# Performance work log

Hardware: AMD Instinct MI355X
Metric: run time of the kernel (lower is better)

## Reference

```python
import jax, jax.numpy as jnp
import numpy as np

N_NODES = 100000
N_EDGES = 1600000
DROP_P = 0.5  # F.dropout default, training=True by default in the source
LRELU_SLOPE = 0.01
EPS = 1e-12


def setup_inputs() -> dict:
    key = jax.random.key(0)
    ks = jax.random.split(key, 8)
    x = jax.random.normal(ks[0], (N_NODES, 64), dtype=jnp.float32)
    edge_index = jax.random.randint(ks[1], (2, N_EDGES), 0, N_NODES, dtype=jnp.int64)
    s = 1.0 / np.sqrt(64)
    W1_l = jax.random.uniform(ks[2], (64, 32), jnp.float32, -s, s)
    W1_r = jax.random.uniform(ks[3], (64, 32), jnp.float32, -s, s)
    b1 = jnp.zeros((32,), jnp.float32)
    s2 = 1.0 / np.sqrt(32)
    W2_l = jax.random.uniform(ks[4], (32, 64), jnp.float32, -s2, s2)
    W2_r = jax.random.uniform(ks[5], (32, 64), jnp.float32, -s2, s2)
    b2 = jnp.zeros((64,), jnp.float32)
    return {"x": x, "edge_index": edge_index, "W1_l": W1_l, "b1": b1,
            "W1_r": W1_r, "W2_l": W2_l, "b2": b2, "W2_r": W2_r}


def _sage_conv(x, src, dst, W_l, b, W_r, n):
    # mean aggregation of source features onto destinations (PyG SAGEConv)
    msg = x[src]                                                 # [E, d]
    agg = jax.ops.segment_sum(msg, dst, num_segments=n)          # [N, d]
    cnt = jax.ops.segment_sum(jnp.ones((src.shape[0],), x.dtype), dst, num_segments=n)
    mean = agg / jnp.maximum(cnt, 1.0)[:, None]
    return mean @ W_l + b + x @ W_r


def _dropout(x, key):
    keep = jax.random.bernoulli(key, 1.0 - DROP_P, x.shape)
    return jnp.where(keep, x / (1.0 - DROP_P), 0.0).astype(x.dtype)


def reference(x, edge_index, W1_l, b1, W1_r, W2_l, b2, W2_r):
    n = x.shape[0]
    src, dst = edge_index[0], edge_index[1]
    dk = jax.random.split(jax.random.key(42), 2)
    h = _sage_conv(x, src, dst, W1_l, b1, W1_r, n)
    h = jax.nn.leaky_relu(h, LRELU_SLOPE)
    h = _dropout(h, dk[0])
    h = _sage_conv(h, src, dst, W2_l, b2, W2_r, n)
    h = _dropout(h, dk[1])
    norm = jnp.sqrt(jnp.sum(h * h, axis=1, keepdims=True))
    return h / jnp.maximum(norm, EPS)
```

## Files before the change

### kernel.cpp

```cpp
#include <hip/hip_runtime.h>

#define N_NODES 100000
#define N_EDGES 1600000
#define NPB 32
#define NB (N_NODES / NPB)
#define CAP 704
#define NCC 49
#define CAPA 34816
#define NFB 64
#define BPC 16
#define N16 (N_NODES * 16)
#define GHB 6250

typedef float v2f __attribute__((ext_vector_type(2)));

struct U2 { unsigned a, b; };

__host__ __device__ constexpr U2 tf2x32(unsigned k0, unsigned k1, unsigned c0, unsigned c1) {
  unsigned ks2 = k0 ^ k1 ^ 0x1BD11BDAu;
  unsigned x0 = c0 + k0, x1 = c1 + k1;
#define TFR(r) { x0 += x1; x1 = (x1 << (r)) | (x1 >> (32 - (r))); x1 ^= x0; }
  TFR(13) TFR(15) TFR(26) TFR(6)
  x0 += k1;  x1 += ks2 + 1u;
  TFR(17) TFR(29) TFR(16) TFR(24)
  x0 += ks2; x1 += k0 + 2u;
  TFR(13) TFR(15) TFR(26) TFR(6)
  x0 += k0;  x1 += k1 + 3u;
  TFR(17) TFR(29) TFR(16) TFR(24)
  x0 += k1;  x1 += ks2 + 4u;
  TFR(13) TFR(15) TFR(26) TFR(6)
  x0 += ks2; x1 += k0 + 5u;
#undef TFR
  return U2{x0, x1};
}

constexpr U2 DK0 = tf2x32(0u, 42u, 0u, 0u);
constexpr U2 DK1 = tf2x32(0u, 42u, 0u, 1u);

__device__ __forceinline__ bool keep_bit(unsigned k0, unsigned k1, unsigned j) {
  U2 w = tf2x32(k0, k1, 0u, j);
  return ((w.a ^ w.b) >> 31) == 0u;
}

__device__ __forceinline__ unsigned short f2bf(float f) {
  unsigned u = __float_as_uint(f);
  u += 0x7FFFu + ((u >> 16) & 1u);
  return (unsigned short)(u >> 16);
}
__device__ __forceinline__ v2f up2(unsigned r) {
  v2f v;
  v.x = __uint_as_float(r << 16);
  v.y = __uint_as_float(r & 0xFFFF0000u);
  return v;
}

__global__ __launch_bounds__(256, 4) void k_transform1(
    const float* __restrict__ x, const float* __restrict__ Wl,
    const float* __restrict__ Wr, unsigned short* __restrict__ xlbh,
    float* __restrict__ xr) {
  __shared__ __align__(16) float rv[4][64];
  int lane = threadIdx.x & 63;
  int wv = (threadIdx.x >> 6) & 3;
  const float* W = (lane < 32) ? Wl : Wr;
  int c = lane & 31;
  float w[64];
#pragma unroll
  for (int k = 0; k < 64; ++k) w[k] = W[k * 32 + c];
  int wid0 = (int)((blockIdx.x * blockDim.x + threadIdx.x) >> 6);
  int wstride = (int)((gridDim.x * blockDim.x) >> 6);
  for (int wid = wid0; wid < N_NODES; wid += wstride) {
    float xv = x[wid * 64 + lane];
    asm volatile("s_waitcnt lgkmcnt(0)" ::: "memory");
    rv[wv][lane] = xv;
    asm volatile("s_waitcnt lgkmcnt(0)" ::: "memory");
    v2f s0 = {0.f, 0.f}, s1 = {0.f, 0.f};
#pragma unroll
    for (int k = 0; k < 64; k += 4) {
      float4 r = *(const float4*)&rv[wv][k];
      v2f w0; w0.x = w[k + 0]; w0.y = w[k + 1];
      v2f w1; w1.x = w[k + 2]; w1.y = w[k + 3];
      v2f p0; p0.x = r.x; p0.y = r.y;
      v2f p1; p1.x = r.z; p1.y = r.w;
      s0 += p0 * w0;
      s1 += p1 * w1;
    }
    float s = (s0.x + s0.y) + (s1.x + s1.y);
    if (lane < 32) xlbh[(size_t)(c >> 4) * N16 + wid * 16 + (c & 15)] = f2bf(s);
    else           xr[wid * 32 + c] = s;
  }
}

__global__ __launch_bounds__(256) void k_binA(
    const int* __restrict__ src, const int* __restrict__ dst,
    int* __restrict__ curA, unsigned* __restrict__ bufA) {
  __shared__ int hist[NCC];
  __shared__ int offsL[NCC + 1];
  __shared__ int baseL[NCC];
  __shared__ int place[NCC];
  __shared__ unsigned stag[2048];
  __shared__ unsigned char cellb[2048];
  int t = threadIdx.x;
  for (long long start = (long long)blockIdx.x * 2048; start < N_EDGES;
       start += (long long)gridDim.x * 2048) {
    int n = (int)min((long long)2048, (long long)N_EDGES - start);
    for (int i = t; i < NCC; i += 256) hist[i] = 0;
    __syncthreads();
    unsigned pv[8]; int pc[8];
#pragma unroll
    for (int i = 0; i < 8; ++i) {
      int idx = t + i * 256;
      if (idx < n) {
        int d = dst[start + idx];
        int s = src[start + idx];
        int cc = d >> 11;
        pc[i] = cc;
        pv[i] = (unsigned)s | ((unsigned)(d & 2047) << 17);
        atomicAdd(&hist[cc], 1);
      } else pc[i] = -1;
    }
    __syncthreads();
    if (t < 64) {
      int lane = t;
      int v = (lane < NCC) ? hist[lane] : 0;
      int x = v;
#pragma unroll
      for (int o = 1; o < 64; o <<= 1) {
        int y = __shfl_up(x, o, 64);
        if (lane >= o) x += y;
      }
      if (lane < NCC) {
        offsL[lane] = x - v;
        place[lane] = 0;
        if (v > 0) baseL[lane] = atomicAdd(&curA[lane], v);
      }
      if (lane == NCC - 1) offsL[NCC] = x;
    }
    __syncthreads();
#pragma unroll
    for (int i = 0; i < 8; ++i) {
      if (pc[i] >= 0) {
        int p = atomicAdd(&place[pc[i]], 1);
        int sl = offsL[pc[i]] + p;
        stag[sl] = pv[i];
        cellb[sl] = (unsigned char)pc[i];
      }
    }
    __syncthreads();
    for (int s2 = t; s2 < n; s2 += 256) {
      int cell = cellb[s2];
      int pos = baseL[cell] + (s2 - offsL[cell]);
      if (pos < CAPA) bufA[(size_t)cell * CAPA + pos] = stag[s2];
    }
    __syncthreads();
  }
}

__global__ __launch_bounds__(256) void k_binB(
    const unsigned* __restrict__ bufA, const int* __restrict__ curA,
    int* __restrict__ cur, unsigned* __restrict__ buf) {
  __shared__ int hist[NFB];
  __shared__ int offsL[NFB + 1];
  __shared__ int baseL[NFB];
  __shared__ int place[NFB];
  __shared__ unsigned stag[2048];
  __shared__ unsigned char cellb[2048];
  int cellc = blockIdx.x / BPC;
  int slice = blockIdx.x % BPC;
  int t = threadIdx.x;
  int cnt = min(curA[cellc], CAPA);
  const unsigned* in = bufA + (size_t)cellc * CAPA;
  for (int start = slice * 2048; start < cnt; start += BPC * 2048) {
    int n = min(2048, cnt - start);
    for (int i = t; i < NFB; i += 256) hist[i] = 0;
    __syncthreads();
    unsigned pv[8]; int pb[8];
#pragma unroll
    for (int i = 0; i < 8; ++i) {
      int idx = t + i * 256;
      if (idx < n) {
        unsigned w = in[start + idx];
        int dlow = (int)(w >> 17);
        int fb = dlow >> 5;
        pb[i] = fb;
        pv[i] = (w & 0x1FFFFu) | ((unsigned)(dlow & 31) << 17);
        atomicAdd(&hist[fb], 1);
      } else pb[i] = -1;
    }
    __syncthreads();
    if (t < 64) {
      int lane = t;
      int v = hist[lane];
      int x = v;
#pragma unroll
      for (int o = 1; o < 64; o <<= 1) {
        int y = __shfl_up(x, o, 64);
        if (lane >= o) x += y;
      }
      offsL[lane] = x - v;
      place[lane] = 0;
      if (v > 0) baseL[lane] = atomicAdd(&cur[cellc * NFB + lane], v);
      if (lane == 63) offsL[NFB] = x;
    }
    __syncthreads();
#pragma unroll
    for (int i = 0; i < 8; ++i) {
      if (pb[i] >= 0) {
        int p = atomicAdd(&place[pb[i]], 1);
        int sl = offsL[pb[i]] + p;
        stag[sl] = pv[i];
        cellb[sl] = (unsigned char)pb[i];
      }
    }
    __syncthreads();
    for (int s2 = t; s2 < n; s2 += 256) {
      int fb = cellb[s2];
      int pos = baseL[fb] + (s2 - offsL[fb]);
      if (pos < CAP) buf[(size_t)(cellc * NFB + fb) * CAP + pos] = stag[s2];
    }
    __syncthreads();
  }
}

__global__ __launch_bounds__(1024) void k_bscan(
    const int* __restrict__ cur, int* __restrict__ bbase) {
  __shared__ int warp_sums[16];
  __shared__ int s_running;
  int t = threadIdx.x;
  int lane = t & 63, w = t >> 6;
  if (t == 0) s_running = 0;
  __syncthreads();
  for (int base = 0; base < NB; base += 1024) {
    int i = base + t;
    int v = (i < NB) ? min(cur[i], CAP) : 0;
    int x = v;
#pragma unroll
    for (int o = 1; o < 64; o <<= 1) {
      int y = __shfl_up(x, o, 64);
      if (lane >= o) x += y;
    }
    if (lane == 63) warp_sums[w] = x;
    __syncthreads();
    if (w == 0) {
      int ws = (lane < 16) ? warp_sums[lane] : 0;
#pragma unroll
      for (int o = 1; o < 16; o <<= 1) {
        int y = __shfl_up(ws, o, 64);
        if (lane >= o) ws += y;
      }
      if (lane < 16) warp_sums[lane] = ws;
    }
    __syncthreads();
    int incl = x + (w > 0 ? warp_sums[w - 1] : 0);
    int excl = s_running + incl - v;
    if (i < NB) bbase[i] = excl;
    __syncthreads();
    if (t == 1023) s_running += incl;
    __syncthreads();
  }
}

__global__ __launch_bounds__(256) void k_bfill(
    const unsigned* __restrict__ buf, const int* __restrict__ cur,
    const int* __restrict__ bbase, int* __restrict__ deg,
    int* __restrict__ offs, int* __restrict__ eidx) {
  __shared__ int ncnt[NPB];
  __shared__ int ncur[NPB];
  __shared__ unsigned sbuf[CAP];
  int b = blockIdx.x, t = threadIdx.x;
  if (t < NPB) ncnt[t] = 0;
  __syncthreads();
  int nb = min(cur[b], CAP);
  const unsigned* bb = buf + (size_t)b * CAP;
  for (int slot = t; slot < nb; slot += 256) {
    unsigned w = bb[slot];
    sbuf[slot] = w;
    atomicAdd(&ncnt[w >> 17], 1);
  }
  __syncthreads();
  if (t < 64) {
    int lane = t;
    int c = (lane < NPB) ? ncnt[lane] : 0;
    int x = c;
#pragma unroll
    for (int o = 1; o < 32; o <<= 1) {
      int y = __shfl_up(x, o, 64);
      if (lane >= o) x += y;
    }
    if (lane < NPB) {
      int excl = x - c;
      ncur[lane] = excl;
      int gn = b * NPB + lane;
      deg[gn] = c;
      offs[gn] = bbase[b] + excl;
    }
  }
  __syncthreads();
  int base = bbase[b];
  for (int slot = t; slot < nb; slot += 256) {
    unsigned w = sbuf[slot];
    int p = atomicAdd(&ncur[w >> 17], 1);
    eidx[base + p] = (int)(w & 0x1FFFF);
  }
}

__global__ __launch_bounds__(256) void k_gather1(
    const unsigned short* __restrict__ xlbh, const float* __restrict__ xr,
    const int* __restrict__ offs, const int* __restrict__ deg,
    const int* __restrict__ eidx, const float* __restrict__ b1,
    unsigned short* __restrict__ hpbh) {
  int bb = blockIdx.x;
  int G = 0, nb = bb;
  if (nb >= GHB) { G = 1; nb -= GHB; }
  int tid = threadIdx.x;
  int lane = tid & 63;
  int node = nb * 16 + (tid >> 4);
  int g = (tid >> 2) & 3;
  int ch = tid & 3;
  int c = tid & 15;
  int col = G * 16 + c;
  int off = offs[node];
  int dg = deg[node];
  float xr_v = xr[node * 32 + col];
  float b1_v = b1[col];
  const uint2* H = (const uint2*)(xlbh + (size_t)G * N16);
  v2f acc01 = {0.f, 0.f}, acc23 = {0.f, 0.f};
  int k = 0;
  for (; k + 8 <= dg; k += 8) {
    int s0 = eidx[off + k + g];
    int s1 = eidx[off + k + 4 + g];
    uint2 r0 = H[s0 * 4 + ch];
    uint2 r1 = H[s1 * 4 + ch];
    acc01 += up2(r0.x); acc23 += up2(r0.y);
    acc01 += up2(r1.x); acc23 += up2(r1.y);
  }
  for (; k < dg; k += 4) {
    if (k + g < dg) {
      int s = eidx[off + k + g];
      uint2 r = H[s * 4 + ch];
      acc01 += up2(r.x); acc23 += up2(r.y);
    }
  }
  float a0 = acc01.x, a1 = acc01.y, a2 = acc23.x, a3 = acc23.y;
  a0 += __shfl_xor(a0, 4, 64); a0 += __shfl_xor(a0, 8, 64);
  a1 += __shfl_xor(a1, 4, 64); a1 += __shfl_xor(a1, 8, 64);
  a2 += __shfl_xor(a2, 4, 64); a2 += __shfl_xor(a2, 8, 64);
  a3 += __shfl_xor(a3, 4, 64); a3 += __shfl_xor(a3, 8, 64);
  int srcl = (lane & 48) + (c >> 2);
  float t0 = __shfl(a0, srcl, 64);
  float t1 = __shfl(a1, srcl, 64);
  float t2 = __shfl(a2, srcl, 64);
  float t3 = __shfl(a3, srcl, 64);
  int sub = lane & 3;
  float val = (sub == 0) ? t0 : (sub == 1) ? t1 : (sub == 2) ? t2 : t3;
  float inv = 1.0f / fmaxf((float)dg, 1.0f);
  int j = node * 32 + col;
  float v = val * inv + b1_v + xr_v;
  v = (v > 0.f) ? v : 0.01f * v;
  float h = keep_bit(DK0.a, DK0.b, (unsigned)j) ? 2.0f * v : 0.0f;
  hpbh[(size_t)G * N16 + node * 16 + c] = f2bf(h);
}

__global__ __launch_bounds__(256) void k_gather2(
    const unsigned short* __restrict__ hpbh, const int* __restrict__ offs,
    const int* __restrict__ deg, const int* __restrict__ eidx,
    float* __restrict__ aggh) {
  int bb = blockIdx.x;
  int G = 0, nb = bb;
  if (nb >= GHB) { G = 1; nb -= GHB; }
  int tid = threadIdx.x;
  int lane = tid & 63;
  int node = nb * 16 + (tid >> 4);
  int g = (tid >> 2) & 3;
  int ch = tid & 3;
  int c = tid & 15;
  int off = offs[node];
  int dg = deg[node];
  const uint2* H = (const uint2*)(hpbh + (size_t)G * N16);
  v2f acc01 = {0.f, 0.f}, acc23 = {0.f, 0.f};
  int k = 0;
  for (; k + 8 <= dg; k += 8) {
    int s0 = eidx[off + k + g];
    int s1 = eidx[off + k + 4 + g];
    uint2 r0 = H[s0 * 4 + ch];
    uint2 r1 = H[s1 * 4 + ch];
    acc01 += up2(r0.x); acc23 += up2(r0.y);
    acc01 += up2(r1.x); acc23 += up2(r1.y);
  }
  for (; k < dg; k += 4) {
    if (k + g < dg) {
      int s = eidx[off + k + g];
      uint2 r = H[s * 4 + ch];
      acc01 += up2(r.x); acc23 += up2(r.y);
    }
  }
  float a0 = acc01.x, a1 = acc01.y, a2 = acc23.x, a3 = acc23.y;
  a0 += __shfl_xor(a0, 4, 64); a0 += __shfl_xor(a0, 8, 64);
  a1 += __shfl_xor(a1, 4, 64); a1 += __shfl_xor(a1, 8, 64);
  a2 += __shfl_xor(a2, 4, 64); a2 += __shfl_xor(a2, 8, 64);
  a3 += __shfl_xor(a3, 4, 64); a3 += __shfl_xor(a3, 8, 64);
  int srcl = (lane & 48) + (c >> 2);
  float t0 = __shfl(a0, srcl, 64);
  float t1 = __shfl(a1, srcl, 64);
  float t2 = __shfl(a2, srcl, 64);
  float t3 = __shfl(a3, srcl, 64);
  int sub = lane & 3;
  float val = (sub == 0) ? t0 : (sub == 1) ? t1 : (sub == 2) ? t2 : t3;
  float inv = 1.0f / fmaxf((float)dg, 1.0f);
  aggh[(size_t)G * N16 + node * 16 + c] = val * inv;
}

__global__ __launch_bounds__(256, 4) void k_out2(
    const unsigned short* __restrict__ hpbh, const float* __restrict__ aggh,
    const float* __restrict__ W2l, const float* __restrict__ b2,
    const float* __restrict__ W2r, float* __restrict__ out) {
  __shared__ __align__(16) float rv[4][64];
  int lane = threadIdx.x & 63;
  int wv = (threadIdx.x >> 6) & 3;
  float wl[32], wr[32];
#pragma unroll
  for (int kk = 0; kk < 32; ++kk) {
    wl[kk] = W2l[kk * 64 + lane];
    wr[kk] = W2r[kk * 64 + lane];
  }
  float bias = b2[lane];
  int wid0 = (int)((blockIdx.x * blockDim.x + threadIdx.x) >> 6);
  int wstride = (int)((gridDim.x * blockDim.x) >> 6);
  for (int wid = wid0; wid < N_NODES; wid += wstride) {
    asm volatile("s_waitcnt lgkmcnt(0)" ::: "memory");
    if (lane < 8) {
      const float* ap = aggh + ((lane < 4) ? 0 : (size_t)N16) + wid * 16 + (lane & 3) * 4;
      float4 v = *(const float4*)ap;
      *(float4*)&rv[wv][lane * 4] = v;
    } else if (lane < 16) {
      const uint2* Hp = (const uint2*)(hpbh + ((lane < 12) ? 0 : (size_t)N16));
      uint2 o = Hp[wid * 4 + (lane & 3)];
      float4 v;
      v.x = __uint_as_float(o.x << 16);
      v.y = __uint_as_float(o.x & 0xFFFF0000u);
      v.z = __uint_as_float(o.y << 16);
      v.w = __uint_as_float(o.y & 0xFFFF0000u);
      *(float4*)&rv[wv][32 + (lane - 8) * 4] = v;
    }
    asm volatile("s_waitcnt lgkmcnt(0)" ::: "memory");
    v2f sa = {0.f, 0.f}, sb = {0.f, 0.f};
#pragma unroll
    for (int kk = 0; kk < 32; kk += 4) {
      float4 r1 = *(const float4*)&rv[wv][kk];
      float4 r2 = *(const float4*)&rv[wv][32 + kk];
      v2f w0; w0.x = wl[kk + 0]; w0.y = wl[kk + 1];
      v2f w1; w1.x = wl[kk + 2]; w1.y = wl[kk + 3];
      v2f u0; u0.x = wr[kk + 0]; u0.y = wr[kk + 1];
      v2f u1; u1.x = wr[kk + 2]; u1.y = wr[kk + 3];
      v2f p0; p0.x = r1.x; p0.y = r1.y;
      v2f p1; p1.x = r1.z; p1.y = r1.w;
      v2f q0; q0.x = r2.x; q0.y = r2.y;
      v2f q1; q1.x = r2.z; q1.y = r2.w;
      sa += p0 * w0;  sa += p1 * w1;
      sb += q0 * u0;  sb += q1 * u1;
    }
    float v = (sa.x + sa.y) + (sb.x + sb.y) + bias;
    unsigned j = (unsigned)(wid * 64 + lane);
    float d = keep_bit(DK1.a, DK1.b, j) ? 2.0f * v : 0.0f;
    float ss = d * d;
#pragma unroll
    for (int o = 32; o > 0; o >>= 1) ss += __shfl_xor(ss, o, 64);
    float scale = 1.0f / fmaxf(sqrtf(ss), 1e-12f);
    out[j] = d * scale;
  }
}

extern "C" void kernel_launch(void* const* d_in, const int* in_sizes, int n_in,
                              void* d_out, int out_size, void* d_ws, size_t ws_size,
                              hipStream_t stream) {
  const float* x   = (const float*)d_in[0];
  const int*   ei  = (const int*)d_in[1];
  const float* W1l = (const float*)d_in[2];
  const float* b1  = (const float*)d_in[3];
  const float* W1r = (const float*)d_in[4];
  const float* W2l = (const float*)d_in[5];
  const float* b2  = (const float*)d_in[6];
  const float* W2r = (const float*)d_in[7];
  float* out = (float*)d_out;

  const int* src = ei;
  const int* dst = ei + N_EDGES;

  const size_t F32 = (size_t)N_NODES * 32;
  char* w = (char*)d_ws;
  unsigned* bufA = (unsigned*)w;
  float* xr      = (float*)w;
  float* aggh    = (float*)w;
  w += F32 * sizeof(float);
  unsigned* buf  = (unsigned*)w;
  unsigned short* xlbh = (unsigned short*)w;
  unsigned short* hpbh = xlbh + 2 * (size_t)N16;
  w += F32 * 2 * sizeof(unsigned short);
  int* curA  = (int*)w; w += NCC * sizeof(int);
  int* cur   = (int*)w; w += NB * sizeof(int);
  int* bbase = (int*)w; w += NB * sizeof(int);
  int* deg   = (int*)w; w += N_NODES * sizeof(int);
  int* offs  = (int*)w; w += N_NODES * sizeof(int);
  int* eidx  = (int*)w;

  hipMemsetAsync(curA, 0, (size_t)(NCC + NB) * sizeof(int), stream);

  k_binA<<<(N_EDGES + 2047) / 2048, 256, 0, stream>>>(src, dst, curA, bufA);
  k_binB<<<NCC * BPC, 256, 0, stream>>>(bufA, curA, cur, buf);
  k_bscan<<<1, 1024, 0, stream>>>(cur, bbase);
  k_bfill<<<NB, 256, 0, stream>>>(buf, cur, bbase, deg, offs, eidx);

  k_transform1<<<1024, 256, 0, stream>>>(x, W1l, W1r, xlbh, xr);
  k_gather1<<<2 * GHB, 256, 0, stream>>>(xlbh, xr, offs, deg, eidx, b1, hpbh);
  k_gather2<<<2 * GHB, 256, 0, stream>>>(hpbh, offs, deg, eidx, aggh);
  k_out2<<<1024, 256, 0, stream>>>(hpbh, aggh, W2l, b2, W2r, out);
}
```

Baseline: 272.9 us.

## Precompute dropout masks as bitmasks and use thread-per-node dense transforms

Adds a k_mask kernel that evaluates the Threefry dropout bits for both layers once, packs them into 64-bit ballot words, and also writes transposed copies of the weight matrices. The gather1 and out2 kernels now read these mask words instead of recomputing Threefry per element. transform1 and out2 switch from wave-per-node with LDS staging to thread-per-node, with weights read through uniform (scalar-cached) loads and vectorized row stores. The trade-off is an extra kernel launch, extra mask traffic, and very high register pressure from 64-wide per-thread arrays.

```diff
diff --git a/kernel.cpp b/kernel.cpp
--- a/kernel.cpp
+++ b/kernel.cpp
@@ -11,6 +11,8 @@
 #define BPC 16
 #define N16 (N_NODES * 16)
 #define GHB 6250
+#define M1W 50000
+#define M2W 100000
 
 typedef float v2f __attribute__((ext_vector_type(2)));
 
@@ -54,40 +56,71 @@
   return v;
 }
 
-__global__ __launch_bounds__(256, 4) void k_transform1(
-    const float* __restrict__ x, const float* __restrict__ Wl,
-    const float* __restrict__ Wr, unsigned short* __restrict__ xlbh,
+__global__ __launch_bounds__(256) void k_mask(
+    unsigned long long* __restrict__ msk,
+    const float* __restrict__ W1l, const float* __restrict__ W1r,
+    const float* __restrict__ W2l, const float* __restrict__ W2r,
+    float* __restrict__ wt) {
+  int bid = blockIdx.x, tid = threadIdx.x;
+  if (bid == 0) {
+    for (int i = tid; i < 2048; i += 256) { int c = i >> 6, k = i & 63; wt[i] = W1l[k * 32 + c]; }
+  } else if (bid == 1) {
+    for (int i = tid; i < 2048; i += 256) { int c = i >> 6, k = i & 63; wt[2048 + i] = W1r[k * 32 + c]; }
+  } else if (bid == 2) {
+    for (int i = tid; i < 2048; i += 256) { int c = i >> 5, k = i & 31; wt[4096 + i] = W2l[k * 64 + c]; }
+  } else if (bid == 3) {
+    for (int i = tid; i < 2048; i += 256) { int c = i >> 5, k = i & 31; wt[6144 + i] = W2r[k * 64 + c]; }
+  }
+  int w = (int)((blockIdx.x * blockDim.x + threadIdx.x) >> 6);
+  int lane = threadIdx.x & 63;
+  int nw = (int)((gridDim.x * blockDim.x) >> 6);
+  for (; w < M1W + M2W; w += nw) {
+    unsigned k0, k1, j;
+    if (w < M1W) { k0 = DK0.a; k1 = DK0.b; j = (unsigned)w * 64u + (unsigned)lane; }
+    else { k0 = DK1.a; k1 = DK1.b; j = (unsigned)(w - M1W) * 64u + (unsigned)lane; }
+    unsigned long long bits = __ballot(keep_bit(k0, k1, j));
+    if (lane == 0) msk[w] = bits;
+  }
+}
+
+__global__ __launch_bounds__(256) void k_transform1(
+    const float* __restrict__ x, const float* __restrict__ W1lT,
+    const float* __restrict__ W1rT, unsigned short* __restrict__ xlbh,
     float* __restrict__ xr) {
-  __shared__ __align__(16) float rv[4][64];
-  int lane = threadIdx.x & 63;
-  int wv = (threadIdx.x >> 6) & 3;
-  const float* W = (lane < 32) ? Wl : Wr;
-  int c = lane & 31;
-  float w[64];
-#pragma unroll
-  for (int k = 0; k < 64; ++k) w[k] = W[k * 32 + c];
-  int wid0 = (int)((blockIdx.x * blockDim.x + threadIdx.x) >> 6);
-  int wstride = (int)((gridDim.x * blockDim.x) >> 6);
-  for (int wid = wid0; wid < N_NODES; wid += wstride) {
-    float xv = x[wid * 64 + lane];
-    asm volatile("s_waitcnt lgkmcnt(0)" ::: "memory");
-    rv[wv][lane] = xv;
-    asm volatile("s_waitcnt lgkmcnt(0)" ::: "memory");
-    v2f s0 = {0.f, 0.f}, s1 = {0.f, 0.f};
-#pragma unroll
-    for (int k = 0; k < 64; k += 4) {
-      float4 r = *(const float4*)&rv[wv][k];
-      v2f w0; w0.x = w[k + 0]; w0.y = w[k + 1];
-      v2f w1; w1.x = w[k + 2]; w1.y = w[k + 3];
-      v2f p0; p0.x = r.x; p0.y = r.y;
-      v2f p1; p1.x = r.z; p1.y = r.w;
-      s0 += p0 * w0;
-      s1 += p1 * w1;
-    }
-    float s = (s0.x + s0.y) + (s1.x + s1.y);
-    if (lane < 32) xlbh[(size_t)(c >> 4) * N16 + wid * 16 + (c & 15)] = f2bf(s);
-    else           xr[wid * 32 + c] = s;
-  }
+  int node = blockIdx.x * 256 + threadIdx.x;
+  if (node >= N_NODES) return;
+  float xv[64];
+  const float4* xp = (const float4*)(x + (size_t)node * 64);
+#pragma unroll 16
+  for (int i = 0; i < 16; ++i) ((float4*)xv)[i] = xp[i];
+  float xl[32], xro[32];
+#pragma unroll 32
+  for (int c = 0; c < 32; ++c) {
+    const float* wl = W1lT + c * 64;
+    const float* wr = W1rT + c * 64;
+    float al0 = 0.f, al1 = 0.f, ar0 = 0.f, ar1 = 0.f;
+#pragma unroll 32
+    for (int k = 0; k < 64; k += 2) {
+      al0 += xv[k] * wl[k];     al1 += xv[k + 1] * wl[k + 1];
+      ar0 += xv[k] * wr[k];     ar1 += xv[k + 1] * wr[k + 1];
+    }
+    xl[c] = al0 + al1;
+    xro[c] = ar0 + ar1;
+  }
+  unsigned pk[16];
+#pragma unroll 16
+  for (int i = 0; i < 16; ++i)
+    pk[i] = (unsigned)f2bf(xl[2 * i]) | ((unsigned)f2bf(xl[2 * i + 1]) << 16);
+  uint4* o0 = (uint4*)(xlbh + (size_t)node * 16);
+  uint4* o1 = (uint4*)(xlbh + (size_t)N16 + (size_t)node * 16);
+  o0[0] = make_uint4(pk[0], pk[1], pk[2], pk[3]);
+  o0[1] = make_uint4(pk[4], pk[5], pk[6], pk[7]);
+  o1[0] = make_uint4(pk[8], pk[9], pk[10], pk[11]);
+  o1[1] = make_uint4(pk[12], pk[13], pk[14], pk[15]);
+  float4* xo = (float4*)(xr + (size_t)node * 32);
+#pragma unroll 8
+  for (int i = 0; i < 8; ++i)
+    xo[i] = make_float4(xro[4 * i], xro[4 * i + 1], xro[4 * i + 2], xro[4 * i + 3]);
 }
 
 __global__ __launch_bounds__(256) void k_binA(
@@ -307,6 +340,7 @@
     const unsigned short* __restrict__ xlbh, const float* __restrict__ xr,
     const int* __restrict__ offs, const int* __restrict__ deg,
     const int* __restrict__ eidx, const float* __restrict__ b1,
+    const unsigned long long* __restrict__ msk1,
     unsigned short* __restrict__ hpbh) {
   int bb = blockIdx.x;
   int G = 0, nb = bb;
@@ -322,6 +356,8 @@
   int dg = deg[node];
   float xr_v = xr[node * 32 + col];
   float b1_v = b1[col];
+  unsigned jj = (unsigned)(node * 32 + col);
+  unsigned long long mw = msk1[jj >> 6];
   const uint2* H = (const uint2*)(xlbh + (size_t)G * N16);
   v2f acc01 = {0.f, 0.f}, acc23 = {0.f, 0.f};
   int k = 0;
@@ -353,10 +389,9 @@
   int sub = lane & 3;
   float val = (sub == 0) ? t0 : (sub == 1) ? t1 : (sub == 2) ? t2 : t3;
   float inv = 1.0f / fmaxf((float)dg, 1.0f);
-  int j = node * 32 + col;
   float v = val * inv + b1_v + xr_v;
   v = (v > 0.f) ? v : 0.01f * v;
-  float h = keep_bit(DK0.a, DK0.b, (unsigned)j) ? 2.0f * v : 0.0f;
+  float h = ((mw >> (jj & 63)) & 1ull) ? 2.0f * v : 0.0f;
   hpbh[(size_t)G * N16 + node * 16 + c] = f2bf(h);
 }
 
@@ -409,64 +444,67 @@
   aggh[(size_t)G * N16 + node * 16 + c] = val * inv;
 }
 
-__global__ __launch_bounds__(256, 4) void k_out2(
+__global__ __launch_bounds__(256) void k_out2(
     const unsigned short* __restrict__ hpbh, const float* __restrict__ aggh,
-    const float* __restrict__ W2l, const float* __restrict__ b2,
-    const float* __restrict__ W2r, float* __restrict__ out) {
-  __shared__ __align__(16) float rv[4][64];
-  int lane = threadIdx.x & 63;
-  int wv = (threadIdx.x >> 6) & 3;
-  float wl[32], wr[32];
-#pragma unroll
-  for (int kk = 0; kk < 32; ++kk) {
-    wl[kk] = W2l[kk * 64 + lane];
-    wr[kk] = W2r[kk * 64 + lane];
-  }
-  float bias = b2[lane];
-  int wid0 = (int)((blockIdx.x * blockDim.x + threadIdx.x) >> 6);
-  int wstride = (int)((gridDim.x * blockDim.x) >> 6);
-  for (int wid = wid0; wid < N_NODES; wid += wstride) {
-    asm volatile("s_waitcnt lgkmcnt(0)" ::: "memory");
-    if (lane < 8) {
-      const float* ap = aggh + ((lane < 4) ? 0 : (size_t)N16) + wid * 16 + (lane & 3) * 4;
-      float4 v = *(const float4*)ap;
-      *(float4*)&rv[wv][lane * 4] = v;
-    } else if (lane < 16) {
-      const uint2* Hp = (const uint2*)(hpbh + ((lane < 12) ? 0 : (size_t)N16));
-      uint2 o = Hp[wid * 4 + (lane & 3)];
-      float4 v;
-      v.x = __uint_as_float(o.x << 16);
-      v.y = __uint_as_float(o.x & 0xFFFF0000u);
-      v.z = __uint_as_float(o.y << 16);
-      v.w = __uint_as_float(o.y & 0xFFFF0000u);
-      *(float4*)&rv[wv][32 + (lane - 8) * 4] = v;
-    }
-    asm volatile("s_waitcnt lgkmcnt(0)" ::: "memory");
-    v2f sa = {0.f, 0.f}, sb = {0.f, 0.f};
-#pragma unroll
-    for (int kk = 0; kk < 32; kk += 4) {
-      float4 r1 = *(const float4*)&rv[wv][kk];
-      float4 r2 = *(const float4*)&rv[wv][32 + kk];
-      v2f w0; w0.x = wl[kk + 0]; w0.y = wl[kk + 1];
-      v2f w1; w1.x = wl[kk + 2]; w1.y = wl[kk + 3];
-      v2f u0; u0.x = wr[kk + 0]; u0.y = wr[kk + 1];
-      v2f u1; u1.x = wr[kk + 2]; u1.y = wr[kk + 3];
-      v2f p0; p0.x = r1.x; p0.y = r1.y;
-      v2f p1; p1.x = r1.z; p1.y = r1.w;
-      v2f q0; q0.x = r2.x; q0.y = r2.y;
-      v2f q1; q1.x = r2.z; q1.y = r2.w;
-      sa += p0 * w0;  sa += p1 * w1;
-      sb += q0 * u0;  sb += q1 * u1;
-    }
-    float v = (sa.x + sa.y) + (sb.x + sb.y) + bias;
-    unsigned j = (unsigned)(wid * 64 + lane);
-    float d = keep_bit(DK1.a, DK1.b, j) ? 2.0f * v : 0.0f;
-    float ss = d * d;
-#pragma unroll
-    for (int o = 32; o > 0; o >>= 1) ss += __shfl_xor(ss, o, 64);
-    float scale = 1.0f / fmaxf(sqrtf(ss), 1e-12f);
-    out[j] = d * scale;
-  }
+    const float* __restrict__ W2lT, const float* __restrict__ b2,
+    const float* __restrict__ W2rT, const unsigned long long* __restrict__ msk2,
+    float* __restrict__ out) {
+  int node = blockIdx.x * 256 + threadIdx.x;
+  if (node >= N_NODES) return;
+  float ag[32];
+  const float4* a0 = (const float4*)(aggh + (size_t)node * 16);
+  const float4* a1 = (const float4*)(aggh + (size_t)N16 + (size_t)node * 16);
+#pragma unroll 4
+  for (int i = 0; i < 4; ++i) ((float4*)ag)[i] = a0[i];
+#pragma unroll 4
+  for (int i = 0; i < 4; ++i) ((float4*)(ag + 16))[i] = a1[i];
+  const uint4* h0 = (const uint4*)(hpbh + (size_t)node * 16);
+  const uint4* h1 = (const uint4*)(hpbh + (size_t)N16 + (size_t)node * 16);
+  uint4 ua = h0[0], ub = h0[1], uc = h1[0], ud = h1[1];
+  unsigned long long mw = msk2[node];
+  float hf[32];
+  {
+    v2f t;
+    t = up2(ua.x); hf[0] = t.x;  hf[1] = t.y;
+    t = up2(ua.y); hf[2] = t.x;  hf[3] = t.y;
+    t = up2(ua.z); hf[4] = t.x;  hf[5] = t.y;
+    t = up2(ua.w); hf[6] = t.x;  hf[7] = t.y;
+    t = up2(ub.x); hf[8] = t.x;  hf[9] = t.y;
+    t = up2(ub.y); hf[10] = t.x; hf[11] = t.y;
+    t = up2(ub.z); hf[12] = t.x; hf[13] = t.y;
+    t = up2(ub.w); hf[14] = t.x; hf[15] = t.y;
+    t = up2(uc.x); hf[16] = t.x; hf[17] = t.y;
+    t = up2(uc.y); hf[18] = t.x; hf[19] = t.y;
+    t = up2(uc.z); hf[20] = t.x; hf[21] = t.y;
+    t = up2(uc.w); hf[22] = t.x; hf[23] = t.y;
+    t = up2(ud.x); hf[24] = t.x; hf[25] = t.y;
+    t = up2(ud.y); hf[26] = t.x; hf[27] = t.y;
+    t = up2(ud.z); hf[28] = t.x; hf[29] = t.y;
+    t = up2(ud.w); hf[30] = t.x; hf[31] = t.y;
+  }
+  float d[64];
+  float ss = 0.f;
+#pragma unroll 64
+  for (int c = 0; c < 64; ++c) {
+    const float* wl = W2lT + c * 32;
+    const float* wr = W2rT + c * 32;
+    float s0 = 0.f, s1 = 0.f;
+#pragma unroll 32
+    for (int k = 0; k < 32; ++k) {
+      s0 += ag[k] * wl[k];
+      s1 += hf[k] * wr[k];
+    }
+    float v = s0 + s1 + b2[c];
+    float dd = ((mw >> c) & 1ull) ? 2.0f * v : 0.0f;
+    d[c] = dd;
+    ss += dd * dd;
+  }
+  float scale = 1.0f / fmaxf(sqrtf(ss), 1e-12f);
+  float4* op = (float4*)(out + (size_t)node * 64);
+#pragma unroll 16
+  for (int i = 0; i < 16; ++i)
+    op[i] = make_float4(d[4 * i] * scale, d[4 * i + 1] * scale,
+                        d[4 * i + 2] * scale, d[4 * i + 3] * scale);
 }
 
 extern "C" void kernel_launch(void* const* d_in, const int* in_sizes, int n_in,
@@ -500,17 +538,25 @@
   int* bbase = (int*)w; w += NB * sizeof(int);
   int* deg   = (int*)w; w += N_NODES * sizeof(int);
   int* offs  = (int*)w; w += N_NODES * sizeof(int);
-  int* eidx  = (int*)w;
+  int* eidx  = (int*)w; w += (size_t)N_EDGES * sizeof(int);
+  unsigned long long* msk = (unsigned long long*)w;
+  w += (size_t)(M1W + M2W) * sizeof(unsigned long long);
+  float* wt = (float*)w;
+  float* W1lT = wt;
+  float* W1rT = wt + 2048;
+  float* W2lT = wt + 4096;
+  float* W2rT = wt + 6144;
 
   hipMemsetAsync(curA, 0, (size_t)(NCC + NB) * sizeof(int), stream);
 
+  k_mask<<<2048, 256, 0, stream>>>(msk, W1l, W1r, W2l, W2r, wt);
   k_binA<<<(N_EDGES + 2047) / 2048, 256, 0, stream>>>(src, dst, curA, bufA);
   k_binB<<<NCC * BPC, 256, 0, stream>>>(bufA, curA, cur, buf);
   k_bscan<<<1, 1024, 0, stream>>>(cur, bbase);
   k_bfill<<<NB, 256, 0, stream>>>(buf, cur, bbase, deg, offs, eidx);
 
-  k_transform1<<<1024, 256, 0, stream>>>(x, W1l, W1r, xlbh, xr);
-  k_gather1<<<2 * GHB, 256, 0, stream>>>(xlbh, xr, offs, deg, eidx, b1, hpbh);
+  k_transform1<<<(N_NODES + 255) / 256, 256, 0, stream>>>(x, W1lT, W1rT, xlbh, xr);
+  k_gather1<<<2 * GHB, 256, 0, stream>>>(xlbh, xr, offs, deg, eidx, b1, msk, hpbh);
   k_gather2<<<2 * GHB, 256, 0, stream>>>(hpbh, offs, deg, eidx, aggh);
-  k_out2<<<1024, 256, 0, stream>>>(hpbh, aggh, W2l, b2, W2r, out);
-}
+  k_out2<<<(N_NODES + 255) / 256, 256, 0, stream>>>(hpbh, aggh, W2lT, b2, W2rT, msk + M1W, out);
+}
```

Result: slower. 336.0 us (+23.1%).

## Fuse layer-2 gather into output kernel and prefetch edge indices via shuffles

Applied to the files above, without the earlier changes.

Merges the second-layer neighbor gather into the output transform kernel, with one wavefront per node gathering both feature halves and reducing across the wave. This removes the intermediate aggregate buffer and one kernel launch. Both gather kernels now load up to 16 or 64 edge indices with one coalesced read and broadcast them by shuffle instead of re-reading the index array per step. The cost is that W2 weights are reloaded per node rather than held in registers, and the fused kernel has lower parallelism per node.

```diff
diff --git a/kernel.cpp b/kernel.cpp
--- a/kernel.cpp
+++ b/kernel.cpp
@@ -322,16 +322,26 @@
   int dg = deg[node];
   float xr_v = xr[node * 32 + col];
   float b1_v = b1[col];
+  int sidx = eidx[(dg > 0) ? (off + min(c, dg - 1)) : 0];
+  int qb = lane & 48;
   const uint2* H = (const uint2*)(xlbh + (size_t)G * N16);
   v2f acc01 = {0.f, 0.f}, acc23 = {0.f, 0.f};
+  int kmax = min(dg, 16);
   int k = 0;
-  for (; k + 8 <= dg; k += 8) {
-    int s0 = eidx[off + k + g];
-    int s1 = eidx[off + k + 4 + g];
-    uint2 r0 = H[s0 * 4 + ch];
-    uint2 r1 = H[s1 * 4 + ch];
+  for (; k + 8 <= kmax; k += 8) {
+    int i0 = __shfl(sidx, qb + k + g, 64);
+    int i1 = __shfl(sidx, qb + k + 4 + g, 64);
+    uint2 r0 = H[i0 * 4 + ch];
+    uint2 r1 = H[i1 * 4 + ch];
     acc01 += up2(r0.x); acc23 += up2(r0.y);
     acc01 += up2(r1.x); acc23 += up2(r1.y);
+  }
+  for (; k < kmax; k += 4) {
+    int i = __shfl(sidx, qb + min(k + g, kmax - 1), 64);
+    if (k + g < kmax) {
+      uint2 r = H[i * 4 + ch];
+      acc01 += up2(r.x); acc23 += up2(r.y);
+    }
   }
   for (; k < dg; k += 4) {
     if (k + g < dg) {
@@ -345,7 +355,7 @@
   a1 += __shfl_xor(a1, 4, 64); a1 += __shfl_xor(a1, 8, 64);
   a2 += __shfl_xor(a2, 4, 64); a2 += __shfl_xor(a2, 8, 64);
   a3 += __shfl_xor(a3, 4, 64); a3 += __shfl_xor(a3, 8, 64);
-  int srcl = (lane & 48) + (c >> 2);
+  int srcl = qb + (c >> 2);
   float t0 = __shfl(a0, srcl, 64);
   float t1 = __shfl(a1, srcl, 64);
   float t2 = __shfl(a2, srcl, 64);
@@ -360,113 +370,103 @@
   hpbh[(size_t)G * N16 + node * 16 + c] = f2bf(h);
 }
 
-__global__ __launch_bounds__(256) void k_gather2(
+__global__ __launch_bounds__(256) void k_out(
     const unsigned short* __restrict__ hpbh, const int* __restrict__ offs,
     const int* __restrict__ deg, const int* __restrict__ eidx,
-    float* __restrict__ aggh) {
-  int bb = blockIdx.x;
-  int G = 0, nb = bb;
-  if (nb >= GHB) { G = 1; nb -= GHB; }
-  int tid = threadIdx.x;
-  int lane = tid & 63;
-  int node = nb * 16 + (tid >> 4);
-  int g = (tid >> 2) & 3;
-  int ch = tid & 3;
-  int c = tid & 15;
-  int off = offs[node];
-  int dg = deg[node];
-  const uint2* H = (const uint2*)(hpbh + (size_t)G * N16);
-  v2f acc01 = {0.f, 0.f}, acc23 = {0.f, 0.f};
-  int k = 0;
-  for (; k + 8 <= dg; k += 8) {
-    int s0 = eidx[off + k + g];
-    int s1 = eidx[off + k + 4 + g];
-    uint2 r0 = H[s0 * 4 + ch];
-    uint2 r1 = H[s1 * 4 + ch];
-    acc01 += up2(r0.x); acc23 += up2(r0.y);
-    acc01 += up2(r1.x); acc23 += up2(r1.y);
-  }
-  for (; k < dg; k += 4) {
-    if (k + g < dg) {
-      int s = eidx[off + k + g];
-      uint2 r = H[s * 4 + ch];
-      acc01 += up2(r.x); acc23 += up2(r.y);
-    }
-  }
-  float a0 = acc01.x, a1 = acc01.y, a2 = acc23.x, a3 = acc23.y;
-  a0 += __shfl_xor(a0, 4, 64); a0 += __shfl_xor(a0, 8, 64);
-  a1 += __shfl_xor(a1, 4, 64); a1 += __shfl_xor(a1, 8, 64);
-  a2 += __shfl_xor(a2, 4, 64); a2 += __shfl_xor(a2, 8, 64);
-  a3 += __shfl_xor(a3, 4, 64); a3 += __shfl_xor(a3, 8, 64);
-  int srcl = (lane & 48) + (c >> 2);
-  float t0 = __shfl(a0, srcl, 64);
-  float t1 = __shfl(a1, srcl, 64);
-  float t2 = __shfl(a2, srcl, 64);
-  float t3 = __shfl(a3, srcl, 64);
-  int sub = lane & 3;
-  float val = (sub == 0) ? t0 : (sub == 1) ? t1 : (sub == 2) ? t2 : t3;
-  float inv = 1.0f / fmaxf((float)dg, 1.0f);
-  aggh[(size_t)G * N16 + node * 16 + c] = val * inv;
-}
-
-__global__ __launch_bounds__(256, 4) void k_out2(
-    const unsigned short* __restrict__ hpbh, const float* __restrict__ aggh,
     const float* __restrict__ W2l, const float* __restrict__ b2,
     const float* __restrict__ W2r, float* __restrict__ out) {
   __shared__ __align__(16) float rv[4][64];
+  int wid = (int)((blockIdx.x * blockDim.x + threadIdx.x) >> 6);
   int lane = threadIdx.x & 63;
   int wv = (threadIdx.x >> 6) & 3;
-  float wl[32], wr[32];
-#pragma unroll
-  for (int kk = 0; kk < 32; ++kk) {
-    wl[kk] = W2l[kk * 64 + lane];
-    wr[kk] = W2r[kk * 64 + lane];
-  }
+  if (wid >= N_NODES) return;
+  int g = lane >> 2;
+  int ch = lane & 3;
+  int off = offs[wid];
+  int dg = deg[wid];
+  const uint2* T0 = (const uint2*)hpbh;
+  const uint2* T1 = (const uint2*)(hpbh + (size_t)N16);
+  uint2 own0 = T0[wid * 4 + ch];
+  uint2 own1 = T1[wid * 4 + ch];
   float bias = b2[lane];
-  int wid0 = (int)((blockIdx.x * blockDim.x + threadIdx.x) >> 6);
-  int wstride = (int)((gridDim.x * blockDim.x) >> 6);
-  for (int wid = wid0; wid < N_NODES; wid += wstride) {
-    asm volatile("s_waitcnt lgkmcnt(0)" ::: "memory");
-    if (lane < 8) {
-      const float* ap = aggh + ((lane < 4) ? 0 : (size_t)N16) + wid * 16 + (lane & 3) * 4;
-      float4 v = *(const float4*)ap;
-      *(float4*)&rv[wv][lane * 4] = v;
-    } else if (lane < 16) {
-      const uint2* Hp = (const uint2*)(hpbh + ((lane < 12) ? 0 : (size_t)N16));
-      uint2 o = Hp[wid * 4 + (lane & 3)];
-      float4 v;
-      v.x = __uint_as_float(o.x << 16);
-      v.y = __uint_as_float(o.x & 0xFFFF0000u);
-      v.z = __uint_as_float(o.y << 16);
-      v.w = __uint_as_float(o.y & 0xFFFF0000u);
-      *(float4*)&rv[wv][32 + (lane - 8) * 4] = v;
-    }
-    asm volatile("s_waitcnt lgkmcnt(0)" ::: "memory");
-    v2f sa = {0.f, 0.f}, sb = {0.f, 0.f};
-#pragma unroll
-    for (int kk = 0; kk < 32; kk += 4) {
-      float4 r1 = *(const float4*)&rv[wv][kk];
-      float4 r2 = *(const float4*)&rv[wv][32 + kk];
-      v2f w0; w0.x = wl[kk + 0]; w0.y = wl[kk + 1];
-      v2f w1; w1.x = wl[kk + 2]; w1.y = wl[kk + 3];
-      v2f u0; u0.x = wr[kk + 0]; u0.y = wr[kk + 1];
-      v2f u1; u1.x = wr[kk + 2]; u1.y = wr[kk + 3];
-      v2f p0; p0.x = r1.x; p0.y = r1.y;
-      v2f p1; p1.x = r1.z; p1.y = r1.w;
-      v2f q0; q0.x = r2.x; q0.y = r2.y;
-      v2f q1; q1.x = r2.z; q1.y = r2.w;
-      sa += p0 * w0;  sa += p1 * w1;
-      sb += q0 * u0;  sb += q1 * u1;
-    }
-    float v = (sa.x + sa.y) + (sb.x + sb.y) + bias;
-    unsigned j = (unsigned)(wid * 64 + lane);
-    float d = keep_bit(DK1.a, DK1.b, j) ? 2.0f * v : 0.0f;
-    float ss = d * d;
-#pragma unroll
-    for (int o = 32; o > 0; o >>= 1) ss += __shfl_xor(ss, o, 64);
-    float scale = 1.0f / fmaxf(sqrtf(ss), 1e-12f);
-    out[j] = d * scale;
-  }
+  int sidx = eidx[(dg > 0) ? (off + min(lane, dg - 1)) : 0];
+  float inv = 1.0f / fmaxf((float)dg, 1.0f);
+  int kmax = min(dg, 64);
+
+#define GATHER_PHASE(T, DEST) { \
+    v2f acc01 = {0.f, 0.f}, acc23 = {0.f, 0.f}; \
+    int k = 0; \
+    for (; k + 16 <= kmax; k += 16) { \
+      int i = __shfl(sidx, k + g, 64); \
+      uint2 r = T[i * 4 + ch]; \
+      acc01 += up2(r.x); acc23 += up2(r.y); \
+    } \
+    for (; k < kmax; k += 16) { \
+      int i = __shfl(sidx, min(k + g, kmax - 1), 64); \
+      if (k + g < kmax) { \
+        uint2 r = T[i * 4 + ch]; \
+        acc01 += up2(r.x); acc23 += up2(r.y); \
+      } \
+    } \
+    for (; k < dg; k += 16) { \
+      if (k + g < dg) { \
+        int s = eidx[off + k + g]; \
+        uint2 r = T[s * 4 + ch]; \
+        acc01 += up2(r.x); acc23 += up2(r.y); \
+      } \
+    } \
+    float a0 = acc01.x, a1 = acc01.y, a2 = acc23.x, a3 = acc23.y; \
+    a0 += __shfl_xor(a0, 4, 64); a0 += __shfl_xor(a0, 8, 64); \
+    a0 += __shfl_xor(a0, 16, 64); a0 += __shfl_xor(a0, 32, 64); \
+    a1 += __shfl_xor(a1, 4, 64); a1 += __shfl_xor(a1, 8, 64); \
+    a1 += __shfl_xor(a1, 16, 64); a1 += __shfl_xor(a1, 32, 64); \
+    a2 += __shfl_xor(a2, 4, 64); a2 += __shfl_xor(a2, 8, 64); \
+    a2 += __shfl_xor(a2, 16, 64); a2 += __shfl_xor(a2, 32, 64); \
+    a3 += __shfl_xor(a3, 4, 64); a3 += __shfl_xor(a3, 8, 64); \
+    a3 += __shfl_xor(a3, 16, 64); a3 += __shfl_xor(a3, 32, 64); \
+    if (lane < 4) { \
+      float4 v; \
+      v.x = a0 * inv; v.y = a1 * inv; v.z = a2 * inv; v.w = a3 * inv; \
+      *(float4*)&rv[wv][(DEST) + lane * 4] = v; \
+    } }
+
+  GATHER_PHASE(T0, 0)
+  GATHER_PHASE(T1, 16)
+#undef GATHER_PHASE
+  if (lane >= 8 && lane < 12) {
+    v2f lo = up2(own0.x), hi = up2(own0.y);
+    float4 v; v.x = lo.x; v.y = lo.y; v.z = hi.x; v.w = hi.y;
+    *(float4*)&rv[wv][32 + (lane - 8) * 4] = v;
+  } else if (lane >= 12 && lane < 16) {
+    v2f lo = up2(own1.x), hi = up2(own1.y);
+    float4 v; v.x = lo.x; v.y = lo.y; v.z = hi.x; v.w = hi.y;
+    *(float4*)&rv[wv][48 + (lane - 12) * 4] = v;
+  }
+  asm volatile("s_waitcnt lgkmcnt(0)" ::: "memory");
+  v2f sa = {0.f, 0.f}, sb = {0.f, 0.f};
+#pragma unroll
+  for (int kk = 0; kk < 32; kk += 4) {
+    float4 r1 = *(const float4*)&rv[wv][kk];
+    float4 r2 = *(const float4*)&rv[wv][32 + kk];
+    v2f w0; w0.x = W2l[(kk + 0) * 64 + lane]; w0.y = W2l[(kk + 1) * 64 + lane];
+    v2f w1; w1.x = W2l[(kk + 2) * 64 + lane]; w1.y = W2l[(kk + 3) * 64 + lane];
+    v2f u0; u0.x = W2r[(kk + 0) * 64 + lane]; u0.y = W2r[(kk + 1) * 64 + lane];
+    v2f u1; u1.x = W2r[(kk + 2) * 64 + lane]; u1.y = W2r[(kk + 3) * 64 + lane];
+    v2f p0; p0.x = r1.x; p0.y = r1.y;
+    v2f p1; p1.x = r1.z; p1.y = r1.w;
+    v2f q0; q0.x = r2.x; q0.y = r2.y;
+    v2f q1; q1.x = r2.z; q1.y = r2.w;
+    sa += p0 * w0;  sa += p1 * w1;
+    sb += q0 * u0;  sb += q1 * u1;
+  }
+  float v = (sa.x + sa.y) + (sb.x + sb.y) + bias;
+  unsigned j = (unsigned)(wid * 64 + lane);
+  float d = keep_bit(DK1.a, DK1.b, j) ? 2.0f * v : 0.0f;
+  float ss = d * d;
+#pragma unroll
+  for (int o = 32; o > 0; o >>= 1) ss += __shfl_xor(ss, o, 64);
+  float scale = 1.0f / fmaxf(sqrtf(ss), 1e-12f);
+  out[j] = d * scale;
 }
 
 extern "C" void kernel_launch(void* const* d_in, const int* in_sizes, int n_in,
@@ -489,7 +489,6 @@
   char* w = (char*)d_ws;
   unsigned* bufA = (unsigned*)w;
   float* xr      = (float*)w;
-  float* aggh    = (float*)w;
   w += F32 * sizeof(float);
   unsigned* buf  = (unsigned*)w;
   unsigned short* xlbh = (unsigned short*)w;
@@ -511,6 +510,5 @@
 
   k_transform1<<<1024, 256, 0, stream>>>(x, W1l, W1r, xlbh, xr);
   k_gather1<<<2 * GHB, 256, 0, stream>>>(xlbh, xr, offs, deg, eidx, b1, hpbh);
-  k_gather2<<<2 * GHB, 256, 0, stream>>>(hpbh, offs, deg, eidx, aggh);
-  k_out2<<<1024, 256, 0, stream>>>(hpbh, aggh, W2l, b2, W2r, out);
-}
+  k_out<<<(N_NODES + 3) / 4, 256, 0, stream>>>(hpbh, offs, deg, eidx, W2l, b2, W2r, out);
+}
```

Measured after the change: 273.8 us. No clear change (+0.3%).
